# Optimization experiments

Hardware: AMD Instinct MI355X
Metric: run time of the kernel (lower is better)

Reference implementation:

```python
import jax, jax.numpy as jnp
import numpy as np

N = 100000      # num nodes
E = 1600000     # num edges
NFEAT = 512
NHID = 256
NCLASS = 32
K = 10
ALPHA = 0.1


def setup_inputs() -> dict:
    key = jax.random.key(0)
    ks = jax.random.split(key, 6)
    x = jax.random.normal(ks[0], (N, NFEAT), dtype=jnp.float32)
    edge_index = jax.random.randint(ks[1], (2, E), 0, N, dtype=jnp.int32)
    edge_attr = jax.random.uniform(ks[2], (E,), dtype=jnp.float32)
    # Linear params (Kaiming-ish scale)
    W_start = jax.random.normal(ks[3], (NFEAT, NHID), dtype=jnp.float32) * np.float32(1.0 / np.sqrt(NFEAT))
    b_start = jnp.zeros((NHID,), jnp.float32)
    W_end = jax.random.normal(ks[4], (NHID, NCLASS), dtype=jnp.float32) * np.float32(1.0 / np.sqrt(NHID))
    b_end = jnp.zeros((NCLASS,), jnp.float32)
    # GPR 'PPR' init coefficients: temp[k] = alpha*(1-alpha)^k, temp[K] = (1-alpha)^K
    temp = (ALPHA * (1.0 - ALPHA) ** np.arange(K + 1)).astype(np.float32)
    temp[-1] = np.float32((1.0 - ALPHA) ** K)
    temp = jnp.asarray(temp)
    return {"x": x, "edge_attr": edge_attr, "W_start": W_start, "b_start": b_start,
            "W_end": W_end, "b_end": b_end, "temp": temp, "edge_index": edge_index}


def gcn_norm(edge_index, edge_weight, num_nodes):
    # add self loops with weight 1 (PyG default fill_value=1)
    loop = jnp.arange(num_nodes, dtype=edge_index.dtype)
    ei = jnp.concatenate([edge_index, jnp.stack([loop, loop])], axis=1)   # [2, E+N]
    ew = jnp.concatenate([edge_weight, jnp.ones((num_nodes,), edge_weight.dtype)])
    row, col = ei[0], ei[1]
    deg = jax.ops.segment_sum(ew, col, num_segments=num_nodes)            # [N]
    dis = jnp.where(deg > 0, jax.lax.rsqrt(jnp.where(deg > 0, deg, 1.0)), 0.0)
    norm = dis[row] * ew * dis[col]                                       # [E+N]
    return ei, norm


def reference(x, edge_attr, W_start, b_start, W_end, b_end, temp, edge_index):
    # MLP front-end (eval mode: dropout is identity)
    h = jax.nn.relu(x @ W_start + b_start)        # [N, NHID]
    h = jax.nn.relu(h @ W_end + b_end)            # [N, NCLASS]
    ei, norm = gcn_norm(edge_index, edge_attr, N)
    row, col = ei[0], ei[1]
    hidden = h * temp[0]
    xk = h
    for k in range(K):
        # SpMM: gather messages norm * x[row], scatter-add at col
        xk = jax.ops.segment_sum(norm[:, None] * xk[row], col, num_segments=N)
        hidden = hidden + temp[k + 1] * xk
    return hidden
```

## Files before the change

### kernel.cpp

```cpp
#include <hip/hip_runtime.h>

typedef __attribute__((ext_vector_type(8))) short short8;
typedef __attribute__((ext_vector_type(4))) float f32x4;
typedef unsigned long long u64;

constexpr int NN = 100000;
constexpr int EE = 1600000;
constexpr int NF = 512;
constexpr int NH = 256;
constexpr int NC = 32;
constexpr int KP = 10;

__device__ __forceinline__ unsigned short f2bf(float f) {
  unsigned int u = __float_as_uint(f);
  u += 0x7FFFu + ((u >> 16) & 1u);
  return (unsigned short)(u >> 16);
}
__device__ __forceinline__ float bf2f(unsigned short s) {
  return __uint_as_float(((unsigned int)s) << 16);
}
__device__ __forceinline__ int padc(int c) { return (c + 7) & ~7; }

__device__ __forceinline__ short8 cvt8(float4 a0, float4 a1) {
  union { unsigned int u[4]; short8 s; } r;
  asm("v_cvt_pk_bf16_f32 %0, %1, %2" : "=v"(r.u[0]) : "v"(a0.x), "v"(a0.y));
  asm("v_cvt_pk_bf16_f32 %0, %1, %2" : "=v"(r.u[1]) : "v"(a0.z), "v"(a0.w));
  asm("v_cvt_pk_bf16_f32 %0, %1, %2" : "=v"(r.u[2]) : "v"(a1.x), "v"(a1.y));
  asm("v_cvt_pk_bf16_f32 %0, %1, %2" : "=v"(r.u[3]) : "v"(a1.z), "v"(a1.w));
  return r.s;
}

__device__ __forceinline__ void block_sync_lds() {
  asm volatile("s_waitcnt lgkmcnt(0)" ::: "memory");
  __builtin_amdgcn_s_barrier();
}

__global__ void convwb_kernel(const float* __restrict__ Ws, const float* __restrict__ We,
                              unsigned short* __restrict__ Wt, unsigned short* __restrict__ Web) {
  int idx = blockIdx.x * 256 + threadIdx.x;
  if (idx < 131072) {
    int col = idx >> 9, k = idx & 511;
    Wt[idx] = f2bf(Ws[(size_t)k * NH + col]);
  } else {
    int j = idx - 131072;
    int col = j >> 8, k = j & 255;
    Web[j] = f2bf(We[(size_t)k * NC + col]);
  }
}

__global__ __launch_bounds__(256, 3) void gemm1_kernel(
    const float* __restrict__ X, const unsigned short* __restrict__ Wt,
    const float* __restrict__ bias, unsigned short* __restrict__ H) {
  constexpr int PAD = 36;
  __shared__ __align__(16) unsigned short Asm[2][128 * PAD];
  __shared__ __align__(16) unsigned short Bsm[2][128 * PAD];
  const int tid = threadIdx.x;
  const int lane = tid & 63;
  const int wave = tid >> 6;
  const int wm = wave >> 1, wn = wave & 1;
  const int l15 = lane & 15, kq = lane >> 4;
  const int m0 = (blockIdx.x >> 1) * 128;
  const int n0 = (blockIdx.x & 1) * 128;

  const int arl0 = tid >> 2, aq = tid & 3;
  int ar0 = m0 + arl0; if (ar0 >= NN) ar0 = NN - 1;
  int ar1 = m0 + arl0 + 64; if (ar1 >= NN) ar1 = NN - 1;
  const float* aptr0 = X + (size_t)ar0 * NF + aq * 8;
  const float* aptr1 = X + (size_t)ar1 * NF + aq * 8;
  const int awr0 = arl0 * PAD + aq * 8;
  const int awr1 = awr0 + 64 * PAD;
  const int bcl = tid >> 1, bh = tid & 1;
  const unsigned short* bptr = Wt + (size_t)(n0 + bcl) * NF + bh * 16;
  const int bwr = bcl * PAD + bh * 16;

  f32x4 acc[4][4];
#pragma unroll
  for (int m = 0; m < 4; m++)
#pragma unroll
    for (int n = 0; n < 4; n++) acc[m][n] = (f32x4)0.0f;

  float4 ra[3][4]; short8 rb0[3], rb1[3];

#define LOADR(ks, j) do { \
    ra[j][0] = *reinterpret_cast<const float4*>(aptr0 + (ks) * 32); \
    ra[j][1] = *reinterpret_cast<const float4*>(aptr0 + (ks) * 32 + 4); \
    ra[j][2] = *reinterpret_cast<const float4*>(aptr1 + (ks) * 32); \
    ra[j][3] = *reinterpret_cast<const float4*>(aptr1 + (ks) * 32 + 4); \
    rb0[j] = *reinterpret_cast<const short8*>(bptr + (ks) * 32); \
    rb1[j] = *reinterpret_cast<const short8*>(bptr + (ks) * 32 + 8); \
  } while (0)

#define STAGE(b, j) do { \
    *reinterpret_cast<short8*>(&Asm[b][awr0]) = cvt8(ra[j][0], ra[j][1]); \
    *reinterpret_cast<short8*>(&Asm[b][awr1]) = cvt8(ra[j][2], ra[j][3]); \
    *reinterpret_cast<short8*>(&Bsm[b][bwr]) = rb0[j]; \
    *reinterpret_cast<short8*>(&Bsm[b][bwr + 8]) = rb1[j]; \
  } while (0)

#define COMPUTE(b) do { \
    short8 af[4], bfr[4]; \
    _Pragma("unroll") \
    for (int mi = 0; mi < 4; mi++) \
      af[mi] = *reinterpret_cast<const short8*>(&Asm[b][(wm * 64 + mi * 16 + l15) * PAD + kq * 8]); \
    _Pragma("unroll") \
    for (int ni = 0; ni < 4; ni++) \
      bfr[ni] = *reinterpret_cast<const short8*>(&Bsm[b][(wn * 64 + ni * 16 + l15) * PAD + kq * 8]); \
    _Pragma("unroll") \
    for (int mi = 0; mi < 4; mi++) \
      _Pragma("unroll") \
      for (int ni = 0; ni < 4; ni++) \
        acc[mi][ni] = __builtin_amdgcn_mfma_f32_16x16x32_bf16(af[mi], bfr[ni], acc[mi][ni], 0, 0, 0); \
  } while (0)

  LOADR(0, 0);
  LOADR(1, 1);
  LOADR(2, 2);
  STAGE(0, 0);
  block_sync_lds();

#pragma unroll
  for (int p = 0; p < 16; p++) {
    if (p + 3 < 16) LOADR(p + 3, (p + 3) % 3);
    COMPUTE(p & 1);
    if (p + 1 < 16) STAGE((p + 1) & 1, (p + 1) % 3);
    block_sync_lds();
  }
#undef LOADR
#undef STAGE
#undef COMPUTE

#pragma unroll
  for (int ni = 0; ni < 4; ni++) {
    int col = n0 + wn * 64 + ni * 16 + l15;
    float bsv = bias[col];
#pragma unroll
    for (int mi = 0; mi < 4; mi++) {
      int rb2 = m0 + wm * 64 + mi * 16 + kq * 4;
#pragma unroll
      for (int i = 0; i < 4; i++) {
        int r = rb2 + i;
        if (r < NN) {
          float v = acc[mi][ni][i] + bsv;
          H[(size_t)r * NH + col] = f2bf(v > 0.f ? v : 0.f);
        }
      }
    }
  }
}

__global__ __launch_bounds__(256) void gemm2_kernel(
    const unsigned short* __restrict__ H, const unsigned short* __restrict__ Web,
    const float* __restrict__ be, const float* __restrict__ temp,
    unsigned short* __restrict__ x0b, float* __restrict__ out) {
  const int tid = threadIdx.x;
  const int lane = tid & 63;
  const int wave = tid >> 6;
  const int l15 = lane & 15, kq = lane >> 4;
  const int rbase = blockIdx.x * 64 + wave * 16;
  int rr = rbase + l15; if (rr >= NN) rr = NN - 1;
  const unsigned short* hrow = H + (size_t)rr * NH + kq * 8;
  const unsigned short* wrow = Web + (size_t)l15 * 256 + kq * 8;

  f32x4 acc[2];
  acc[0] = (f32x4)0.0f; acc[1] = (f32x4)0.0f;
#pragma unroll
  for (int ks = 0; ks < 8; ks++) {
    short8 a = *reinterpret_cast<const short8*>(hrow + ks * 32);
    short8 b0 = *reinterpret_cast<const short8*>(wrow + ks * 32);
    short8 b1 = *reinterpret_cast<const short8*>(wrow + 16 * 256 + ks * 32);
    acc[0] = __builtin_amdgcn_mfma_f32_16x16x32_bf16(a, b0, acc[0], 0, 0, 0);
    acc[1] = __builtin_amdgcn_mfma_f32_16x16x32_bf16(a, b1, acc[1], 0, 0, 0);
  }
  const float t0 = temp[0];
#pragma unroll
  for (int nt = 0; nt < 2; nt++) {
    int col = nt * 16 + l15;
    float bv = be[col];
#pragma unroll
    for (int i = 0; i < 4; i++) {
      int row = rbase + kq * 4 + i;
      if (row < NN) {
        float v = acc[nt][i] + bv;
        v = v > 0.f ? v : 0.f;
        x0b[(size_t)row * NC + col] = f2bf(v);
        out[(size_t)row * NC + col] = t0 * v;
      }
    }
  }
}

__global__ void node_init_kernel(u64* dc) {
  int i = blockIdx.x * 256 + threadIdx.x;
  if (i < NN) dc[i] = (1ULL << 44) | (1ULL << 32);
}

__global__ void edge_deg_kernel(const int* __restrict__ ei, const float* __restrict__ ew,
                                u64* dc) {
  int e = blockIdx.x * 256 + threadIdx.x;
  if (e < EE) {
    int col = ei[EE + e];
    u64 v = (1ULL << 44) | (u64)((double)ew[e] * 4294967296.0);
    atomicAdd(&dc[col], v);
  }
}

__global__ void dis_kernel(const u64* __restrict__ dc, float* __restrict__ dis,
                           int* __restrict__ cnt) {
  int i = blockIdx.x * 256 + threadIdx.x;
  if (i < NN) {
    u64 v = dc[i];
    cnt[i] = (int)(v >> 44);
    float deg = (float)((double)(v & 0xFFFFFFFFFFFULL) * (1.0 / 4294967296.0));
    dis[i] = rsqrtf(deg);
  }
}

__global__ void scan1_kernel(const int* __restrict__ cnt, int* bsum) {
  __shared__ int ws[4];
  const int tid = threadIdx.x;
  int base = blockIdx.x * 1024 + tid * 4;
  int s = 0;
#pragma unroll
  for (int j = 0; j < 4; j++) { int i = base + j; if (i < NN) s += padc(cnt[i]); }
  for (int off = 32; off > 0; off >>= 1) s += __shfl_down(s, off);
  if ((tid & 63) == 0) ws[tid >> 6] = s;
  __syncthreads();
  if (tid == 0) bsum[blockIdx.x] = ws[0] + ws[1] + ws[2] + ws[3];
}

__global__ void scan2_kernel(const int* __restrict__ bsum, int* bofs, int* offs) {
  if (threadIdx.x == 0) {
    int run = 0;
    for (int i = 0; i < 98; i++) { bofs[i] = run; run += bsum[i]; }
    offs[NN] = run;
  }
}

__global__ void scan3_kernel(const int* __restrict__ cnt, const int* __restrict__ bofs,
                             int* offs, int* cursor) {
  __shared__ int wsum[4];
  const int tid = threadIdx.x;
  const int lane = tid & 63, wv = tid >> 6;
  int base = blockIdx.x * 1024 + tid * 4;
  int v[4]; int s = 0;
#pragma unroll
  for (int j = 0; j < 4; j++) { int i = base + j; v[j] = (i < NN) ? padc(cnt[i]) : 0; s += v[j]; }
  int incl = s;
  for (int off = 1; off < 64; off <<= 1) {
    int t = __shfl_up(incl, off);
    if (lane >= off) incl += t;
  }
  if (lane == 63) wsum[wv] = incl;
  __syncthreads();
  int woff = bofs[blockIdx.x];
  for (int w = 0; w < wv; w++) woff += wsum[w];
  int excl = woff + incl - s;
#pragma unroll
  for (int j = 0; j < 4; j++) {
    int i = base + j;
    if (i < NN) { offs[i] = excl; cursor[i] = excl; }
    excl += v[j];
  }
}

__global__ void fill_kernel(const int* __restrict__ ei, const float* __restrict__ ew,
                            const float* __restrict__ dis, int* cursor,
                            u64* __restrict__ pk) {
  int t = blockIdx.x * 256 + threadIdx.x;
  if (t < EE) {
    int r = ei[t], c = ei[EE + t];
    int slot = atomicAdd(&cursor[c], 1);
    unsigned int wb = __float_as_uint(dis[r] * ew[t] * dis[c]);
    pk[slot] = (u64)(unsigned int)r | ((u64)wb << 32);
  } else if (t < EE + NN) {
    int i = t - EE;
    int slot = atomicAdd(&cursor[i], 1);
    float d = dis[i];
    unsigned int wb = __float_as_uint(d * d);
    pk[slot] = (u64)(unsigned int)i | ((u64)wb << 32);
  }
}

__global__ void pad_kernel(const int* __restrict__ cursor, const int* __restrict__ offs,
                           u64* __restrict__ pk) {
  int i = blockIdx.x * 256 + threadIdx.x;
  if (i < NN) {
    int j = cursor[i], e = offs[i + 1];
    for (; j < e; j++) pk[j] = 0;
  }
}

__global__ __launch_bounds__(256) void spmm_kernel(
    const int* __restrict__ offs, const u64* __restrict__ pk,
    const unsigned short* __restrict__ xin, unsigned short* __restrict__ xout) {
  const int tid = threadIdx.x;
  const int node = blockIdx.x * 32 + (tid >> 3);
  const int fq = (tid & 7) * 4;
  const int s = offs[node], e = offs[node + 1];
  float a0 = 0.f, a1 = 0.f, a2 = 0.f, a3 = 0.f;
  for (int j = s; j < e; j += 8) {
    ulonglong2 p01 = *reinterpret_cast<const ulonglong2*>(pk + j);
    ulonglong2 p23 = *reinterpret_cast<const ulonglong2*>(pk + j + 2);
    ulonglong2 p45 = *reinterpret_cast<const ulonglong2*>(pk + j + 4);
    ulonglong2 p67 = *reinterpret_cast<const ulonglong2*>(pk + j + 6);
    const u64 p[8] = {p01.x, p01.y, p23.x, p23.y, p45.x, p45.y, p67.x, p67.y};
    u64 q[8];
#pragma unroll
    for (int i = 0; i < 8; i++)
      q[i] = *reinterpret_cast<const u64*>(xin + (size_t)(unsigned int)p[i] * NC + fq);
#pragma unroll
    for (int i = 0; i < 8; i++) {
      const float w = __uint_as_float((unsigned int)(p[i] >> 32));
      a0 += w * bf2f((unsigned short)(q[i]));
      a1 += w * bf2f((unsigned short)(q[i] >> 16));
      a2 += w * bf2f((unsigned short)(q[i] >> 32));
      a3 += w * bf2f((unsigned short)(q[i] >> 48));
    }
  }
  unsigned int lo, hi;
  asm("v_cvt_pk_bf16_f32 %0, %1, %2" : "=v"(lo) : "v"(a0), "v"(a1));
  asm("v_cvt_pk_bf16_f32 %0, %1, %2" : "=v"(hi) : "v"(a2), "v"(a3));
  *reinterpret_cast<u64*>(xout + (size_t)node * NC + fq) =
      (u64)lo | ((u64)hi << 32);
}

__global__ __launch_bounds__(256) void wsum_kernel(
    const unsigned short* __restrict__ S07,
    const unsigned short* __restrict__ S8, const unsigned short* __restrict__ S9,
    float* __restrict__ out, const float* __restrict__ temp) {
  int t8 = blockIdx.x * 256 + threadIdx.x;
  if (t8 >= NN * NC / 8) return;
  const size_t base = (size_t)t8 * 8;
  float s[8];
  float4 o0 = *reinterpret_cast<const float4*>(out + base);
  float4 o1 = *reinterpret_cast<const float4*>(out + base + 4);
  s[0] = o0.x; s[1] = o0.y; s[2] = o0.z; s[3] = o0.w;
  s[4] = o1.x; s[5] = o1.y; s[6] = o1.z; s[7] = o1.w;
#pragma unroll
  for (int k = 0; k < 8; k++) {
    const float tk = temp[k + 1];
    short8 v = *reinterpret_cast<const short8*>(S07 + (size_t)k * NN * NC + base);
#pragma unroll
    for (int t = 0; t < 8; t++) s[t] += tk * bf2f((unsigned short)v[t]);
  }
  {
    const float tk = temp[9];
    short8 v = *reinterpret_cast<const short8*>(S8 + base);
#pragma unroll
    for (int t = 0; t < 8; t++) s[t] += tk * bf2f((unsigned short)v[t]);
  }
  {
    const float tk = temp[10];
    short8 v = *reinterpret_cast<const short8*>(S9 + base);
#pragma unroll
    for (int t = 0; t < 8; t++) s[t] += tk * bf2f((unsigned short)v[t]);
  }
  *reinterpret_cast<float4*>(out + base) = make_float4(s[0], s[1], s[2], s[3]);
  *reinterpret_cast<float4*>(out + base + 4) = make_float4(s[4], s[5], s[6], s[7]);
}

extern "C" void kernel_launch(void* const* d_in, const int* in_sizes, int n_in,
                              void* d_out, int out_size, void* d_ws, size_t ws_size,
                              hipStream_t stream) {
  const float* X    = (const float*)d_in[0];
  const float* EA   = (const float*)d_in[1];
  const float* Ws   = (const float*)d_in[2];
  const float* bs   = (const float*)d_in[3];
  const float* We   = (const float*)d_in[4];
  const float* be   = (const float*)d_in[5];
  const float* temp = (const float*)d_in[6];
  const int*   ei   = (const int*)d_in[7];
  float* out = (float*)d_out;

  size_t off = 0;
  auto alloc = [&](size_t n) { void* p = (char*)d_ws + off; off += (n + 255) & ~(size_t)255; return p; };
  unsigned short* Wt  = (unsigned short*)alloc((size_t)NF * NH * 2);
  unsigned short* Web = (unsigned short*)alloc((size_t)NH * NC * 2);
  unsigned short* H   = (unsigned short*)alloc((size_t)NN * NH * 2);
  unsigned short* x0b = (unsigned short*)alloc((size_t)NN * NC * 2);
  unsigned short* xk8 = (unsigned short*)alloc((size_t)NN * NC * 2);
  unsigned short* xk9 = (unsigned short*)alloc((size_t)NN * NC * 2);
  u64*   dc   = (u64*)alloc((size_t)NN * 8);
  float* dis  = (float*)alloc((size_t)NN * 4);
  int*   cnt  = (int*)alloc((size_t)NN * 4);
  int*   offs = (int*)alloc((size_t)(NN + 1) * 4);
  int*   cursor = (int*)alloc((size_t)NN * 4);
  int*   bsum = (int*)alloc(98 * 4);
  int*   bofs = (int*)alloc(98 * 4);
  u64*   pk   = (u64*)alloc((size_t)(EE + 8 * NN) * 8);

  convwb_kernel<<<544, 256, 0, stream>>>(Ws, We, Wt, Web);
  gemm1_kernel<<<1564, 256, 0, stream>>>(X, Wt, bs, H);
  gemm2_kernel<<<1563, 256, 0, stream>>>(H, Web, be, temp, x0b, out);

  node_init_kernel<<<391, 256, 0, stream>>>(dc);
  edge_deg_kernel<<<6250, 256, 0, stream>>>(ei, EA, dc);
  dis_kernel<<<391, 256, 0, stream>>>(dc, dis, cnt);
  scan1_kernel<<<98, 256, 0, stream>>>(cnt, bsum);
  scan2_kernel<<<1, 64, 0, stream>>>(bsum, bofs, offs);
  scan3_kernel<<<98, 256, 0, stream>>>(cnt, bofs, offs, cursor);
  fill_kernel<<<6641, 256, 0, stream>>>(ei, EA, dis, cursor, pk);
  pad_kernel<<<391, 256, 0, stream>>>(cursor, offs, pk);

  auto slice = [&](int k) -> unsigned short* {
    return (k < 8) ? H + (size_t)k * NN * NC : (k == 8 ? xk8 : xk9);
  };
  const unsigned short* xin = x0b;
  for (int k = 0; k < KP; k++) {
    spmm_kernel<<<3125, 256, 0, stream>>>(offs, pk, xin, slice(k));
    xin = slice(k);
  }
  wsum_kernel<<<1563, 256, 0, stream>>>(H, xk8, xk9, out, temp);
}
```

Baseline: 539.3 us.

## Fuse second MLP GEMM into first GEMM via LDS-staged hidden tile

The first GEMM now computes a full 64x256 hidden tile per block instead of 128x128 tiles, then stages the relu'd bf16 hidden activations through shared memory in two halves and immediately multiplies by W_end to produce x0b and the temp[0]-scaled output. This removes the round trip of the 51 MB bf16 H matrix through global memory and one kernel launch. In exchange, each block now reads the whole weight matrix (256 columns) per 64 rows, so B-operand traffic per output row doubles and the A tile is smaller, which may lower GEMM efficiency.

Result: no change. 537.6 us (-0.3%).

```diff
diff --git a/kernel.cpp b/kernel.cpp
--- a/kernel.cpp
+++ b/kernel.cpp
@@ -50,28 +50,24 @@
 
 __global__ __launch_bounds__(256, 3) void gemm1_kernel(
     const float* __restrict__ X, const unsigned short* __restrict__ Wt,
-    const float* __restrict__ bias, unsigned short* __restrict__ H) {
+    const float* __restrict__ bias, const unsigned short* __restrict__ Web,
+    const float* __restrict__ be, const float* __restrict__ temp,
+    unsigned short* __restrict__ x0b, float* __restrict__ out) {
   constexpr int PAD = 36;
-  __shared__ __align__(16) unsigned short Asm[2][128 * PAD];
-  __shared__ __align__(16) unsigned short Bsm[2][128 * PAD];
+  __shared__ __align__(16) unsigned short Asm[2][64 * PAD];
+  __shared__ __align__(16) unsigned short Bsm[2][256 * PAD];
   const int tid = threadIdx.x;
   const int lane = tid & 63;
-  const int wave = tid >> 6;
-  const int wm = wave >> 1, wn = wave & 1;
+  const int w = tid >> 6;
   const int l15 = lane & 15, kq = lane >> 4;
-  const int m0 = (blockIdx.x >> 1) * 128;
-  const int n0 = (blockIdx.x & 1) * 128;
-
-  const int arl0 = tid >> 2, aq = tid & 3;
-  int ar0 = m0 + arl0; if (ar0 >= NN) ar0 = NN - 1;
-  int ar1 = m0 + arl0 + 64; if (ar1 >= NN) ar1 = NN - 1;
-  const float* aptr0 = X + (size_t)ar0 * NF + aq * 8;
-  const float* aptr1 = X + (size_t)ar1 * NF + aq * 8;
-  const int awr0 = arl0 * PAD + aq * 8;
-  const int awr1 = awr0 + 64 * PAD;
-  const int bcl = tid >> 1, bh = tid & 1;
-  const unsigned short* bptr = Wt + (size_t)(n0 + bcl) * NF + bh * 16;
-  const int bwr = bcl * PAD + bh * 16;
+  const int m0 = blockIdx.x * 64;
+
+  const int arl = tid >> 2, aq = tid & 3;
+  int ar = m0 + arl; if (ar >= NN) ar = NN - 1;
+  const float* aptr = X + (size_t)ar * NF + aq * 8;
+  const int awr = arl * PAD + aq * 8;
+  const unsigned short* bptr = Wt + (size_t)tid * NF;
+  const int bwr = tid * PAD;
 
   f32x4 acc[4][4];
 #pragma unroll
@@ -79,32 +75,33 @@
 #pragma unroll
     for (int n = 0; n < 4; n++) acc[m][n] = (f32x4)0.0f;
 
-  float4 ra[3][4]; short8 rb0[3], rb1[3];
+  float4 ra[3][2]; short8 rb[3][4];
 
 #define LOADR(ks, j) do { \
-    ra[j][0] = *reinterpret_cast<const float4*>(aptr0 + (ks) * 32); \
-    ra[j][1] = *reinterpret_cast<const float4*>(aptr0 + (ks) * 32 + 4); \
-    ra[j][2] = *reinterpret_cast<const float4*>(aptr1 + (ks) * 32); \
-    ra[j][3] = *reinterpret_cast<const float4*>(aptr1 + (ks) * 32 + 4); \
-    rb0[j] = *reinterpret_cast<const short8*>(bptr + (ks) * 32); \
-    rb1[j] = *reinterpret_cast<const short8*>(bptr + (ks) * 32 + 8); \
+    ra[j][0] = *reinterpret_cast<const float4*>(aptr + (ks) * 32); \
+    ra[j][1] = *reinterpret_cast<const float4*>(aptr + (ks) * 32 + 4); \
+    rb[j][0] = *reinterpret_cast<const short8*>(bptr + (ks) * 32); \
+    rb[j][1] = *reinterpret_cast<const short8*>(bptr + (ks) * 32 + 8); \
+    rb[j][2] = *reinterpret_cast<const short8*>(bptr + (ks) * 32 + 16); \
+    rb[j][3] = *reinterpret_cast<const short8*>(bptr + (ks) * 32 + 24); \
   } while (0)
 
 #define STAGE(b, j) do { \
-    *reinterpret_cast<short8*>(&Asm[b][awr0]) = cvt8(ra[j][0], ra[j][1]); \
-    *reinterpret_cast<short8*>(&Asm[b][awr1]) = cvt8(ra[j][2], ra[j][3]); \
-    *reinterpret_cast<short8*>(&Bsm[b][bwr]) = rb0[j]; \
-    *reinterpret_cast<short8*>(&Bsm[b][bwr + 8]) = rb1[j]; \
+    *reinterpret_cast<short8*>(&Asm[b][awr]) = cvt8(ra[j][0], ra[j][1]); \
+    *reinterpret_cast<short8*>(&Bsm[b][bwr]) = rb[j][0]; \
+    *reinterpret_cast<short8*>(&Bsm[b][bwr + 8]) = rb[j][1]; \
+    *reinterpret_cast<short8*>(&Bsm[b][bwr + 16]) = rb[j][2]; \
+    *reinterpret_cast<short8*>(&Bsm[b][bwr + 24]) = rb[j][3]; \
   } while (0)
 
 #define COMPUTE(b) do { \
     short8 af[4], bfr[4]; \
     _Pragma("unroll") \
     for (int mi = 0; mi < 4; mi++) \
-      af[mi] = *reinterpret_cast<const short8*>(&Asm[b][(wm * 64 + mi * 16 + l15) * PAD + kq * 8]); \
+      af[mi] = *reinterpret_cast<const short8*>(&Asm[b][(mi * 16 + l15) * PAD + kq * 8]); \
     _Pragma("unroll") \
     for (int ni = 0; ni < 4; ni++) \
-      bfr[ni] = *reinterpret_cast<const short8*>(&Bsm[b][(wn * 64 + ni * 16 + l15) * PAD + kq * 8]); \
+      bfr[ni] = *reinterpret_cast<const short8*>(&Bsm[b][(w * 64 + ni * 16 + l15) * PAD + kq * 8]); \
     _Pragma("unroll") \
     for (int mi = 0; mi < 4; mi++) \
       _Pragma("unroll") \
@@ -129,58 +126,50 @@
 #undef STAGE
 #undef COMPUTE
 
-#pragma unroll
-  for (int ni = 0; ni < 4; ni++) {
-    int col = n0 + wn * 64 + ni * 16 + l15;
-    float bsv = bias[col];
-#pragma unroll
-    for (int mi = 0; mi < 4; mi++) {
-      int rb2 = m0 + wm * 64 + mi * 16 + kq * 4;
-#pragma unroll
-      for (int i = 0; i < 4; i++) {
-        int r = rb2 + i;
-        if (r < NN) {
-          float v = acc[mi][ni][i] + bsv;
-          H[(size_t)r * NH + col] = f2bf(v > 0.f ? v : 0.f);
-        }
+  unsigned short* Ht = (unsigned short*)Bsm;
+  f32x4 acc2[2];
+  acc2[0] = (f32x4)0.0f; acc2[1] = (f32x4)0.0f;
+  const unsigned short* wrow = Web + (size_t)l15 * 256 + kq * 8;
+#pragma unroll
+  for (int p2 = 0; p2 < 2; p2++) {
+    block_sync_lds();
+    if ((w >> 1) == p2) {
+#pragma unroll
+      for (int ni = 0; ni < 4; ni++) {
+        const int colg = w * 64 + ni * 16 + l15;
+        const float bsv = bias[colg];
+        const int cl = colg - p2 * 128;
+#pragma unroll
+        for (int mi = 0; mi < 4; mi++)
+#pragma unroll
+          for (int i = 0; i < 4; i++) {
+            const int row = mi * 16 + kq * 4 + i;
+            const float v = acc[mi][ni][i] + bsv;
+            Ht[row * 136 + cl] = f2bf(v > 0.f ? v : 0.f);
+          }
       }
     }
-  }
-}
-
-__global__ __launch_bounds__(256) void gemm2_kernel(
-    const unsigned short* __restrict__ H, const unsigned short* __restrict__ Web,
-    const float* __restrict__ be, const float* __restrict__ temp,
-    unsigned short* __restrict__ x0b, float* __restrict__ out) {
-  const int tid = threadIdx.x;
-  const int lane = tid & 63;
-  const int wave = tid >> 6;
-  const int l15 = lane & 15, kq = lane >> 4;
-  const int rbase = blockIdx.x * 64 + wave * 16;
-  int rr = rbase + l15; if (rr >= NN) rr = NN - 1;
-  const unsigned short* hrow = H + (size_t)rr * NH + kq * 8;
-  const unsigned short* wrow = Web + (size_t)l15 * 256 + kq * 8;
-
-  f32x4 acc[2];
-  acc[0] = (f32x4)0.0f; acc[1] = (f32x4)0.0f;
-#pragma unroll
-  for (int ks = 0; ks < 8; ks++) {
-    short8 a = *reinterpret_cast<const short8*>(hrow + ks * 32);
-    short8 b0 = *reinterpret_cast<const short8*>(wrow + ks * 32);
-    short8 b1 = *reinterpret_cast<const short8*>(wrow + 16 * 256 + ks * 32);
-    acc[0] = __builtin_amdgcn_mfma_f32_16x16x32_bf16(a, b0, acc[0], 0, 0, 0);
-    acc[1] = __builtin_amdgcn_mfma_f32_16x16x32_bf16(a, b1, acc[1], 0, 0, 0);
+    block_sync_lds();
+    const unsigned short* hr = Ht + (size_t)(w * 16 + l15) * 136 + kq * 8;
+#pragma unroll
+    for (int ks = 0; ks < 4; ks++) {
+      short8 a  = *reinterpret_cast<const short8*>(hr + ks * 32);
+      short8 b0 = *reinterpret_cast<const short8*>(wrow + p2 * 128 + ks * 32);
+      short8 b1 = *reinterpret_cast<const short8*>(wrow + 16 * 256 + p2 * 128 + ks * 32);
+      acc2[0] = __builtin_amdgcn_mfma_f32_16x16x32_bf16(a, b0, acc2[0], 0, 0, 0);
+      acc2[1] = __builtin_amdgcn_mfma_f32_16x16x32_bf16(a, b1, acc2[1], 0, 0, 0);
+    }
   }
   const float t0 = temp[0];
 #pragma unroll
   for (int nt = 0; nt < 2; nt++) {
-    int col = nt * 16 + l15;
-    float bv = be[col];
+    const int col = nt * 16 + l15;
+    const float bv = be[col];
 #pragma unroll
     for (int i = 0; i < 4; i++) {
-      int row = rbase + kq * 4 + i;
+      const int row = m0 + w * 16 + kq * 4 + i;
       if (row < NN) {
-        float v = acc[nt][i] + bv;
+        float v = acc2[nt][i] + bv;
         v = v > 0.f ? v : 0.f;
         x0b[(size_t)row * NC + col] = f2bf(v);
         out[(size_t)row * NC + col] = t0 * v;
@@ -376,7 +365,7 @@
   auto alloc = [&](size_t n) { void* p = (char*)d_ws + off; off += (n + 255) & ~(size_t)255; return p; };
   unsigned short* Wt  = (unsigned short*)alloc((size_t)NF * NH * 2);
   unsigned short* Web = (unsigned short*)alloc((size_t)NH * NC * 2);
-  unsigned short* H   = (unsigned short*)alloc((size_t)NN * NH * 2);
+  unsigned short* SL  = (unsigned short*)alloc((size_t)NN * NH * 2);
   unsigned short* x0b = (unsigned short*)alloc((size_t)NN * NC * 2);
   unsigned short* xk8 = (unsigned short*)alloc((size_t)NN * NC * 2);
   unsigned short* xk9 = (unsigned short*)alloc((size_t)NN * NC * 2);
@@ -390,8 +379,7 @@
   u64*   pk   = (u64*)alloc((size_t)(EE + 8 * NN) * 8);
 
   convwb_kernel<<<544, 256, 0, stream>>>(Ws, We, Wt, Web);
-  gemm1_kernel<<<1564, 256, 0, stream>>>(X, Wt, bs, H);
-  gemm2_kernel<<<1563, 256, 0, stream>>>(H, Web, be, temp, x0b, out);
+  gemm1_kernel<<<1563, 256, 0, stream>>>(X, Wt, bs, Web, be, temp, x0b, out);
 
   node_init_kernel<<<391, 256, 0, stream>>>(dc);
   edge_deg_kernel<<<6250, 256, 0, stream>>>(ei, EA, dc);
@@ -403,12 +391,12 @@
   pad_kernel<<<391, 256, 0, stream>>>(cursor, offs, pk);
 
   auto slice = [&](int k) -> unsigned short* {
-    return (k < 8) ? H + (size_t)k * NN * NC : (k == 8 ? xk8 : xk9);
+    return (k < 8) ? SL + (size_t)k * NN * NC : (k == 8 ? xk8 : xk9);
   };
   const unsigned short* xin = x0b;
   for (int k = 0; k < KP; k++) {
     spmm_kernel<<<3125, 256, 0, stream>>>(offs, pk, xin, slice(k));
     xin = slice(k);
   }
-  wsum_kernel<<<1563, 256, 0, stream>>>(H, xk8, xk9, out, temp);
-}
+  wsum_kernel<<<1563, 256, 0, stream>>>(SL, xk8, xk9, out, temp);
+}
```
